# Kernel tuning notes

Hardware: AMD Instinct MI355X
Metric: run time of the kernel (lower is better)

Reference implementation:

```python
import jax, jax.numpy as jnp
import numpy as np

N, C, H, W = 2, 4, 112, 112
IGNORE = 0  # HD_IGNORE_CLASS_INDEX


def setup_inputs() -> dict:
    key = jax.random.key(0)
    k1, k2 = jax.random.split(key)
    predictions = jax.random.normal(k1, (N, C, H, W), dtype=jnp.float32)
    labels = jax.random.randint(k2, (N, C, H, W), 0, 2, dtype=jnp.int32)
    return {"predictions": predictions, "labels": labels}


def _pixel_dist_matrix(h, w):
    # Euclidean distance between all pairs of (row, col) pixel coordinates,
    # identical to cdist(argwhere(...), argwhere(...)) restricted by masks.
    rr, cc = jnp.meshgrid(jnp.arange(h, dtype=jnp.float32),
                          jnp.arange(w, dtype=jnp.float32), indexing="ij")
    r = rr.reshape(-1)
    c = cc.reshape(-1)
    return jnp.sqrt((r[:, None] - r[None, :]) ** 2 + (c[:, None] - c[None, :]) ** 2)  # (HW, HW)


def reference(predictions, labels):
    # F.softmax + argmax + one-hot -> per-class boolean prediction masks
    probs = jax.nn.softmax(predictions, axis=1)
    pred_cls = jnp.argmax(probs, axis=1)  # (N, H, W) int

    D = _pixel_dist_matrix(H, W)  # (HW, HW), data-independent

    fhd = jnp.zeros(C + 2, jnp.float32)
    rhd = jnp.zeros(C + 2, jnp.float32)
    mhd = jnp.zeros(C + 2, jnp.float32)

    for b in range(N):
        for j in range(C):
            if j == IGNORE:
                continue
            A = (pred_cls[b] == j).reshape(-1)        # predicted point set mask (HW,)
            Bm = (labels[b, j] == 1).reshape(-1)      # label point set mask (HW,)
            Af = A.astype(jnp.float32)
            Bf = Bm.astype(jnp.float32)
            # forward: mean over A-points of min distance to B-points
            rowmin = jnp.min(jnp.where(Bm[None, :], D, jnp.inf), axis=1)  # (HW,)
            fwd = jnp.sum(rowmin * Af) / jnp.sum(Af)
            # reverse: mean over B-points of min distance to A-points
            colmin = jnp.min(jnp.where(A[:, None], D, jnp.inf), axis=0)   # (HW,)
            rev = jnp.sum(colmin * Bf) / jnp.sum(Bf)
            fhd = fhd.at[j].add(fwd)
            rhd = rhd.at[j].add(rev)
            mhd = mhd.at[j].add(jnp.maximum(fwd, rev))

    def finalize(x):
        x = x.at[:C].divide(jnp.float32(N))
        x = x.at[C].set(jnp.mean(x[:C]))
        x = x.at[C + 1].set(jnp.mean(x[1:C]))
        return x

    return (finalize(mhd), finalize(fhd), finalize(rhd))
```

## Files before the change

kernel.cpp:

```cpp
#include <hip/hip_runtime.h>
#include <hip/hip_bf16.h>
#include <cstdint>
#include <climits>

#define HW 112
#define NPIX (HW*HW)
#define NB 2
#define NC 4
#define HALF_ROWS 56
#define HD_BLKS 24


__global__ __launch_bounds__(128) void prep_kernel(
    const float* __restrict__ pred, const int* __restrict__ labels,
    unsigned long long* __restrict__ masks, unsigned short* __restrict__ gsqbuf,
    unsigned* __restrict__ counter)
{
  int blk = blockIdx.x;
  int b = blk / HW, r = blk % HW;
  int tid = threadIdx.x;
  int lane = tid & 63, wave = tid >> 6;
  int c = tid;

  if (blk == 0 && tid == 0) *counter = 0;

  int cls = 255;
  if (c < HW) {
    const float* p0 = pred + ((size_t)(b*NC)*HW + r)*HW + c;
    float best = p0[0]; cls = 0;
    #pragma unroll
    for (int ch = 1; ch < NC; ch++) {
      float v = p0[(size_t)ch*NPIX];
      if (v > best) { best = v; cls = ch; }
    }
  }

  __shared__ unsigned long long sm[6][2];
  #pragma unroll
  for (int m = 0; m < 3; m++) {
    bool p = (c < HW) && (cls == m + 1);
    unsigned long long bal = __ballot(p);
    if (lane == 0) sm[m][wave] = bal;
  }
  #pragma unroll
  for (int m = 0; m < 3; m++) {
    int lab = (c < HW) ? labels[((size_t)(b*NC + (m+1))*HW + r)*HW + c] : 0;
    bool p = (c < HW) && (lab == 1);
    unsigned long long bal = __ballot(p);
    if (lane == 0) sm[3 + m][wave] = bal;
  }
  __syncthreads();

  if (tid < 12) {
    int m = tid >> 1, w = tid & 1;
    masks[((size_t)(b*6 + m)*HW + r)*2 + w] = sm[m][w];
  }

  for (int item = tid; item < 6*HW; item += 128) {
    int m = item / HW, cc = item % HW;
    unsigned long long lo = sm[m][0], hi = sm[m][1];
    int left, right;
    if (cc < 64) {
      unsigned long long wl = lo & ((2ull << cc) - 1);
      left = wl ? 63 - __clzll(wl) : -1000;
      unsigned long long wr = lo & ~((1ull << cc) - 1);
      right = wr ? __ffsll(wr) - 1 : (hi ? 64 + __ffsll(hi) - 1 : 1000);
    } else {
      int cl = cc - 64;
      unsigned long long wl = hi & ((2ull << cl) - 1);
      left = wl ? 64 + 63 - __clzll(wl) : (lo ? 63 - __clzll(lo) : -1000);
      unsigned long long wr = hi & ~((1ull << cl) - 1);
      right = wr ? 64 + __ffsll(wr) - 1 : 1000;
    }
    int gv = min(min(cc - left, right - cc), 255);
    gsqbuf[(size_t)(b*6 + m)*NPIX + r*HW + cc] = (unsigned short)(gv*gv);
  }
}

__device__ __forceinline__ int g2row(const unsigned short* __restrict__ g2p, int row) {
  return (row >= 0 && row < HW) ? (int)g2p[(size_t)row*HW] : 0x7fff;
}

__global__ __launch_bounds__(1024) void hd_kernel(
    const unsigned long long* __restrict__ masks,
    const unsigned short* __restrict__ gsqbuf,
    float* __restrict__ S, float* __restrict__ Cc,
    unsigned* __restrict__ counter, float* __restrict__ out)
{
  int blk = blockIdx.x;
  int pd = blk >> 1, half = blk & 1;
  int b = pd / 6, k = pd % 6;
  int src = b*6 + (k + 3) % 6;
  int tid = threadIdx.x, lane = tid & 63, wv = tid >> 6;
  int rg = tid / HW, c = tid % HW;

  float sum = 0.f, cf = 0.f;
  if (rg < 8) {
    const unsigned short* g2p = gsqbuf + (size_t)src*NPIX + c;
    int rbase = half*HALF_ROWS + rg*7;
    int vm2 = g2row(g2p, rbase - 2), vm1 = g2row(g2p, rbase - 1);
    int v0  = g2row(g2p, rbase),     vp1 = g2row(g2p, rbase + 1);
    int vp2 = g2row(g2p, rbase + 2);
    #pragma unroll 7
    for (int i = 0; i < 7; i++) {
      int r = rbase + i;
      int best = v0;
      best = min(best, 1 + min(vm1, vp1));
      best = min(best, 4 + min(vm2, vp2));
      if (best > 9) {
        for (int d = 3; d < HW; d++) {
          int dd = d*d;
          if (dd >= best) break;
          int ru = r - d, rd = r + d;
          if (ru >= 0)  best = min(best, dd + (int)g2p[(size_t)ru*HW]);
          if (rd < HW)  best = min(best, dd + (int)g2p[(size_t)rd*HW]);
        }
      }
      unsigned long long wm = masks[((size_t)pd*HW + r)*2 + (c >> 6)];
      if ((wm >> (c & 63)) & 1ull) { sum += sqrtf((float)best); cf += 1.f; }
      vm2 = vm1; vm1 = v0; v0 = vp1; vp1 = vp2; vp2 = g2row(g2p, r + 3);
    }
  }

  #pragma unroll
  for (int off = 32; off; off >>= 1) {
    sum += __shfl_down(sum, off, 64);
    cf  += __shfl_down(cf, off, 64);
  }
  __shared__ float red[32];
  __shared__ int isLast;
  if (lane == 0) { red[wv*2] = sum; red[wv*2 + 1] = cf; }
  __syncthreads();
  if (tid == 0) {
    float Sv = 0.f, Cv = 0.f;
    #pragma unroll
    for (int w = 0; w < 16; w++) { Sv += red[w*2]; Cv += red[w*2 + 1]; }
    atomicExch(&S[blk], Sv);
    atomicExch(&Cc[blk], Cv);
    __threadfence();
    unsigned old = atomicAdd(counter, 1u);
    isLast = (old == HD_BLKS - 1) ? 1 : 0;
  }
  __syncthreads();

  if (isLast) {
    __shared__ float fs[HD_BLKS], fc[HD_BLKS], sacc[24];
    if (tid < HD_BLKS) {
      fs[tid] = atomicAdd(&S[tid], 0.0f);
      fc[tid] = atomicAdd(&Cc[tid], 0.0f);
    }
    __syncthreads();
    if (tid < 12) {
      sacc[tid]      = fs[tid*2] + fs[tid*2 + 1];
      sacc[12 + tid] = fc[tid*2] + fc[tid*2 + 1];
    }
    __syncthreads();
    if (tid == 0) {
      float mhd[6], fhd[6], rhd[6];
      for (int i = 0; i < 6; i++) { mhd[i] = 0.f; fhd[i] = 0.f; rhd[i] = 0.f; }
      for (int bb = 0; bb < 2; bb++)
        for (int j = 1; j < 4; j++) {
          int pf = bb*6 + (j - 1);
          int pr = bb*6 + 3 + (j - 1);
          float fwd = sacc[pf] / sacc[12 + pf];
          float rev = sacc[pr] / sacc[12 + pr];
          fhd[j] += fwd; rhd[j] += rev; mhd[j] += fmaxf(fwd, rev);
        }
      float* arrs[3] = { mhd, fhd, rhd };
      for (int a = 0; a < 3; a++) {
        float* x = arrs[a];
        for (int i = 0; i < 4; i++) x[i] *= 0.5f;
        x[4] = (x[0] + x[1] + x[2] + x[3]) * 0.25f;
        x[5] = (x[1] + x[2] + x[3]) * (1.f / 3.f);
        for (int i = 0; i < 6; i++) out[a*6 + i] = x[i];
      }
    }
  }
}

extern "C" void kernel_launch(void* const* d_in, const int* in_sizes, int n_in,
                              void* d_out, int out_size, void* d_ws, size_t ws_size,
                              hipStream_t stream) {
  const float* pred = (const float*)d_in[0];
  const int* labels = (const int*)d_in[1];
  float* out = (float*)d_out;

  unsigned long long* masks = (unsigned long long*)d_ws;
  unsigned short* gsqbuf = (unsigned short*)((char*)d_ws + 21504);
  float* S  = (float*)((char*)d_ws + 322560);
  float* Cc = (float*)((char*)d_ws + 322656);
  unsigned* counter = (unsigned*)((char*)d_ws + 322752);

  prep_kernel<<<NB*HW, 128, 0, stream>>>(pred, labels, masks, gsqbuf, counter);
  hd_kernel<<<HD_BLKS, 1024, 0, stream>>>(masks, gsqbuf, S, Cc, counter, out);
}
```

Before: 16.98 us.

## Split HD kernel into 168 small blocks with per-pair atomic accumulation

The distance kernel moves from 24 blocks of 1024 threads to 168 blocks of 128 threads, each handling 8 rows of one mask pair, so work is spread across many more CUs. The per-block partial slots are replaced by float atomicAdd into per-pair accumulators, with a two-level counter (per pair, then global) choosing which block finalizes. This aims to cut the serialized per-thread row work and improve occupancy, at the cost of more atomics and non-deterministic float summation order.

```diff
diff --git a/kernel.cpp b/kernel.cpp
--- a/kernel.cpp
+++ b/kernel.cpp
@@ -7,14 +7,14 @@
 #define NPIX (HW*HW)
 #define NB 2
 #define NC 4
-#define HALF_ROWS 56
-#define HD_BLKS 24
+#define CHUNKS 14
+#define HD_GRID (12*CHUNKS)
 
 
 __global__ __launch_bounds__(128) void prep_kernel(
     const float* __restrict__ pred, const int* __restrict__ labels,
     unsigned long long* __restrict__ masks, unsigned short* __restrict__ gsqbuf,
-    unsigned* __restrict__ counter)
+    float* __restrict__ accum)
 {
   int blk = blockIdx.x;
   int b = blk / HW, r = blk % HW;
@@ -22,7 +22,7 @@
   int lane = tid & 63, wave = tid >> 6;
   int c = tid;
 
-  if (blk == 0 && tid == 0) *counter = 0;
+  if (blk == 0 && tid < 37) accum[tid] = 0.f;
 
   int cls = 255;
   if (c < HW) {
@@ -81,28 +81,32 @@
   return (row >= 0 && row < HW) ? (int)g2p[(size_t)row*HW] : 0x7fff;
 }
 
-__global__ __launch_bounds__(1024) void hd_kernel(
+__global__ __launch_bounds__(128) void hd_kernel(
     const unsigned long long* __restrict__ masks,
     const unsigned short* __restrict__ gsqbuf,
-    float* __restrict__ S, float* __restrict__ Cc,
-    unsigned* __restrict__ counter, float* __restrict__ out)
+    float* __restrict__ accum, float* __restrict__ out)
 {
+  float* pdS = accum;
+  float* pdC = accum + 12;
+  unsigned* pdcnt = (unsigned*)(accum + 24);
+  unsigned* gcnt  = (unsigned*)(accum + 36);
+
   int blk = blockIdx.x;
-  int pd = blk >> 1, half = blk & 1;
+  int pd = blk / CHUNKS, chunk = blk % CHUNKS;
   int b = pd / 6, k = pd % 6;
   int src = b*6 + (k + 3) % 6;
   int tid = threadIdx.x, lane = tid & 63, wv = tid >> 6;
-  int rg = tid / HW, c = tid % HW;
+  int c = tid;
+  int rbase = chunk * 8;
 
   float sum = 0.f, cf = 0.f;
-  if (rg < 8) {
+  if (c < HW) {
     const unsigned short* g2p = gsqbuf + (size_t)src*NPIX + c;
-    int rbase = half*HALF_ROWS + rg*7;
     int vm2 = g2row(g2p, rbase - 2), vm1 = g2row(g2p, rbase - 1);
     int v0  = g2row(g2p, rbase),     vp1 = g2row(g2p, rbase + 1);
     int vp2 = g2row(g2p, rbase + 2);
-    #pragma unroll 7
-    for (int i = 0; i < 7; i++) {
+    #pragma unroll 8
+    for (int i = 0; i < 8; i++) {
       int r = rbase + i;
       int best = v0;
       best = min(best, 1 + min(vm1, vp1));
@@ -127,33 +131,27 @@
     sum += __shfl_down(sum, off, 64);
     cf  += __shfl_down(cf, off, 64);
   }
-  __shared__ float red[32];
-  __shared__ int isLast;
+  __shared__ float red[4];
+  __shared__ int doFin;
   if (lane == 0) { red[wv*2] = sum; red[wv*2 + 1] = cf; }
   __syncthreads();
   if (tid == 0) {
-    float Sv = 0.f, Cv = 0.f;
-    #pragma unroll
-    for (int w = 0; w < 16; w++) { Sv += red[w*2]; Cv += red[w*2 + 1]; }
-    atomicExch(&S[blk], Sv);
-    atomicExch(&Cc[blk], Cv);
+    doFin = 0;
+    atomicAdd(&pdS[pd], red[0] + red[2]);
+    atomicAdd(&pdC[pd], red[1] + red[3]);
     __threadfence();
-    unsigned old = atomicAdd(counter, 1u);
-    isLast = (old == HD_BLKS - 1) ? 1 : 0;
+    unsigned pdold = atomicAdd(&pdcnt[pd], 1u);
+    if (pdold == CHUNKS - 1) {
+      unsigned gold = atomicAdd(gcnt, 1u);
+      if (gold == 11) doFin = 1;
+    }
   }
   __syncthreads();
 
-  if (isLast) {
-    __shared__ float fs[HD_BLKS], fc[HD_BLKS], sacc[24];
-    if (tid < HD_BLKS) {
-      fs[tid] = atomicAdd(&S[tid], 0.0f);
-      fc[tid] = atomicAdd(&Cc[tid], 0.0f);
-    }
-    __syncthreads();
-    if (tid < 12) {
-      sacc[tid]      = fs[tid*2] + fs[tid*2 + 1];
-      sacc[12 + tid] = fc[tid*2] + fc[tid*2 + 1];
-    }
+  if (doFin) {
+    __shared__ float sacc[24];
+    if (tid < 12)       sacc[tid]      = atomicAdd(&pdS[tid], 0.0f);
+    else if (tid < 24)  sacc[tid]      = atomicAdd(&pdC[tid - 12], 0.0f);
     __syncthreads();
     if (tid == 0) {
       float mhd[6], fhd[6], rhd[6];
@@ -187,10 +185,8 @@
 
   unsigned long long* masks = (unsigned long long*)d_ws;
   unsigned short* gsqbuf = (unsigned short*)((char*)d_ws + 21504);
-  float* S  = (float*)((char*)d_ws + 322560);
-  float* Cc = (float*)((char*)d_ws + 322656);
-  unsigned* counter = (unsigned*)((char*)d_ws + 322752);
+  float* accum = (float*)((char*)d_ws + 322560);
 
-  prep_kernel<<<NB*HW, 128, 0, stream>>>(pred, labels, masks, gsqbuf, counter);
-  hd_kernel<<<HD_BLKS, 1024, 0, stream>>>(masks, gsqbuf, S, Cc, counter, out);
+  prep_kernel<<<NB*HW, 128, 0, stream>>>(pred, labels, masks, gsqbuf, accum);
+  hd_kernel<<<HD_GRID, 128, 0, stream>>>(masks, gsqbuf, accum, out);
 }
```

New measurement: 18.72 us. 10.3% more time.
